# Kernel optimization log

Measured on AMD Instinct MI355X. Metric: run time of the kernel, lower is better.

The kernel has to match this reference:

```python
import jax, jax.numpy as jnp
import numpy as np

# ---- static hyperparameters (from init_kwargs) ----
N_ORDER = 3
P = N_ORDER + 1                      # nodes per element
N_ELEM = 64
N_NODES = N_ELEM * N_ORDER + 1       # 193
XMIN_IN, XMAX_IN = -1.0, 1.0         # inner layer domain
XMIN_OUT, XMAX_OUT = -3.0, 3.0       # outer layer domain (covers t_ik range)
N_SAMPLES, N_WIDTH, NDIM = 32768, 32, 4

_NODES = np.linspace(-1.0, 1.0, P)   # reference-element nodes


def lagr_bases(xt):
    """Lagrange basis values and 1st/2nd derivatives on the reference element.
    xt: (...,) -> phi, dphi, ddphi each (..., P)."""
    nd = _NODES
    d = xt[..., None] - jnp.asarray(nd, dtype=xt.dtype)  # (..., P), d[...,m] = x - nodes[m]
    phi_l, dphi_l, ddphi_l = [], [], []
    for j in range(P):
        # phi_j = prod_{m!=j} (x - n_m)/(n_j - n_m)
        p = jnp.ones_like(xt)
        for m in range(P):
            if m != j:
                p = p * d[..., m] / float(nd[j] - nd[m])
        phi_l.append(p)
        # dphi_j = sum_{i!=j} 1/(n_j-n_i) * prod_{m!=i,j} (x-n_m)/(n_j-n_m)
        y = jnp.zeros_like(xt)
        for i in range(P):
            if i == j:
                continue
            k = jnp.ones_like(xt) / float(nd[j] - nd[i])
            for m in range(P):
                if m != i and m != j:
                    k = k * d[..., m] / float(nd[j] - nd[m])
            y = y + k
        dphi_l.append(y)
        # ddphi_j = sum_{i!=j} 1/(n_j-n_i) * sum_{m!=i,j} 1/(n_j-n_m) * prod_{n!=i,j,m} (x-n_n)/(n_j-n_n)
        y2 = jnp.zeros_like(xt)
        for i in range(P):
            if i == j:
                continue
            ks = jnp.zeros_like(xt)
            for m in range(P):
                if m == i or m == j:
                    continue
                kp = jnp.ones_like(xt) / float(nd[j] - nd[m])
                for n in range(P):
                    if n != i and n != j and n != m:
                        kp = kp * d[..., n] / float(nd[j] - nd[n])
                ks = ks + kp
            y2 = y2 + ks / float(nd[j] - nd[i])
        ddphi_l.append(y2)
    return (jnp.stack(phi_l, -1), jnp.stack(dphi_l, -1), jnp.stack(ddphi_l, -1))


def layer_transform(x, x_min, x_max, n_nodes, n_elements):
    """Shift to natural coords, pick element by floor-division, map to reference coords."""
    x_shift = (n_nodes - 1) * (x - x_min) / (x_max - x_min)
    id_el = jnp.clip(jnp.floor(x_shift / N_ORDER), 0.0, n_elements - 1)
    nodes_l = (id_el * N_ORDER).astype(jnp.int32)
    x_ref = 2.0 * (x_shift - nodes_l) / N_ORDER - 1.0
    delta = 0.5 * N_ORDER * (x_max - x_min) / (n_nodes - 1)
    return x_ref, nodes_l, delta


def setup_inputs() -> dict:
    key = jax.random.key(0)
    k1, k2, k3 = jax.random.split(key, 3)
    x = jax.random.uniform(k1, (N_SAMPLES, NDIM), dtype=jnp.float32)       # in [x_min, x_max]
    W_in = 0.1 * jax.random.normal(k2, (N_WIDTH, N_NODES, NDIM), dtype=jnp.float32)
    W_out = 0.1 * jax.random.normal(k3, (N_WIDTH, N_NODES), dtype=jnp.float32)
    return {"x": x, "W_in": W_in, "W_out": W_out}


def reference(x, W_in, W_out):
    I, J = x.shape
    K = W_in.shape[0]
    # ---- inner layer: per-(sample,width,dim) local Lagrange basis ----
    xk = jnp.broadcast_to(x[:, None, :], (I, K, J))                        # (I,K,J)
    xt, nodes_l, delta = layer_transform(xk, XMIN_IN, XMAX_IN, N_NODES, N_ELEM)
    phi, dphi, ddphi = lagr_bases(xt)                                      # (I,K,J,P)
    # gather form of scatter + einsum('kpj,ikpj->ik'): sum_p,j W[k, nodes_l+p, j]*phi_local
    node_idx = nodes_l[..., None] + jnp.arange(P)                          # (I,K,J,P)
    kk = jnp.arange(K)[None, :, None, None]
    jj = jnp.arange(J)[None, None, :, None]
    Wg = W_in[kk, node_idx, jj]                                            # (I,K,J,P)
    t = jnp.einsum('ikjp,ikjp->ik', Wg, phi)
    dt = jnp.einsum('ikjp,ikjp->ik', Wg, dphi) / delta
    ddt = jnp.einsum('ikjp,ikjp->ik', Wg, ddphi) / (delta * delta)
    # ---- outer layer on t_ik (already 2D) ----
    xt2, nodes_l2, _ = layer_transform(t, XMIN_OUT, XMAX_OUT, N_NODES, N_ELEM)
    phi2, _, _ = lagr_bases(xt2)                                           # (I,K,P)
    node_idx2 = nodes_l2[..., None] + jnp.arange(P)                        # (I,K,P)
    kk2 = jnp.arange(K)[None, :, None]
    W2g = W_out[kk2, node_idx2]                                            # (I,K,P)
    y = jnp.einsum('ikp,ikp->ik', W2g, phi2)
    return jnp.stack([y, t, dt, ddt], axis=0)                              # (4,I,K)
```

## Files before the change

kernel.cpp:

```cpp
#include <hip/hip_runtime.h>

constexpr int I_SAMPLES = 32768;
constexpr int K_WIDTH   = 32;
constexpr int NNODES    = 193;
constexpr int N_ELEM    = 64;
constexpr int IK        = I_SAMPLES * K_WIDTH;

constexpr int W1_N = 4 * N_ELEM * K_WIDTH;
constexpr int W2_N = N_ELEM * K_WIDTH;

__global__ __launch_bounds__(256) void prep_kernel(
    const float* __restrict__ W_in,
    const float* __restrict__ W_out,
    float4* __restrict__ W1,
    float4* __restrict__ W2)
{
    const int t = blockIdx.x * blockDim.x + threadIdx.x;
    if (t < W1_N) {
        const int k = t & 31;
        const int e = (t >> 5) & 63;
        const int j = t >> 11;
        const int base = (k * NNODES + 3 * e) * 4 + j;
        float4 v;
        v.x = W_in[base + 0 * 4];
        v.y = W_in[base + 1 * 4];
        v.z = W_in[base + 2 * 4];
        v.w = W_in[base + 3 * 4];
        W1[t] = v;
    } else if (t < W1_N + W2_N) {
        const int u = t - W1_N;
        const int k = u & 31;
        const int e = u >> 5;
        const int base = k * NNODES + 3 * e;
        float4 v;
        v.x = W_out[base + 0];
        v.y = W_out[base + 1];
        v.z = W_out[base + 2];
        v.w = W_out[base + 3];
        W2[u] = v;
    }
}

__global__ __launch_bounds__(256) void kann_kernel(
    const float* __restrict__ x,
    const float4* __restrict__ W1,
    const float4* __restrict__ W2,
    float* __restrict__ out)
{
    const int tid = blockIdx.x * blockDim.x + threadIdx.x;
    const int c = tid & 7;
    const int i = tid >> 3;

    const float4 xv = reinterpret_cast<const float4*>(x)[i];
    const float xj[4] = {xv.x, xv.y, xv.z, xv.w};

    const float C3[4] = {-0.5625f,  1.6875f, -1.6875f,  0.5625f};
    const float C2[4] = { 0.5625f, -0.5625f, -0.5625f,  0.5625f};
    const float C1[4] = { 0.0625f, -1.6875f,  1.6875f, -0.0625f};
    const float C0[4] = {-0.0625f,  0.5625f,  0.5625f, -0.0625f};

    float tacc[4] = {0.f, 0.f, 0.f, 0.f};
    float dta[4]  = {0.f, 0.f, 0.f, 0.f};
    float dda[4]  = {0.f, 0.f, 0.f, 0.f};

    #pragma unroll
    for (int j = 0; j < 4; ++j) {
        const float xs = (192.0f * (xj[j] + 1.0f)) / 2.0f;
        float ide = floorf(xs / 3.0f);
        ide = fminf(fmaxf(ide, 0.0f), 63.0f);
        const int e  = (int)ide;
        const int nl = 3 * e;
        const float xr = (2.0f * (xs - (float)nl)) / 3.0f - 1.0f;

        float phi[4], dph[4], ddp[4];
        #pragma unroll
        for (int p = 0; p < 4; ++p) {
            phi[p] = ((C3[p] * xr + C2[p]) * xr + C1[p]) * xr + C0[p];
            dph[p] = (3.0f * C3[p] * xr + 2.0f * C2[p]) * xr + C1[p];
            ddp[p] = 6.0f * C3[p] * xr + 2.0f * C2[p];
        }

        const float4* row = W1 + (j * N_ELEM + e) * K_WIDTH + c;
        #pragma unroll
        for (int q = 0; q < 4; ++q) {
            const float4 w = row[8 * q];
            const float wv[4] = {w.x, w.y, w.z, w.w};
            #pragma unroll
            for (int p = 0; p < 4; ++p) {
                tacc[q] += wv[p] * phi[p];
                dta[q]  += wv[p] * dph[p];
                dda[q]  += wv[p] * ddp[p];
            }
        }
    }

    #pragma unroll
    for (int q = 0; q < 4; ++q) {
        const float t   = tacc[q];
        const float dt  = dta[q] * 64.0f;
        const float ddt = dda[q] * 4096.0f;

        const float xs2 = (192.0f * (t + 3.0f)) / 6.0f;
        float id2 = floorf(xs2 / 3.0f);
        id2 = fminf(fmaxf(id2, 0.0f), 63.0f);
        const int e2  = (int)id2;
        const int nl2 = 3 * e2;
        const float xr2 = (2.0f * (xs2 - (float)nl2)) / 3.0f - 1.0f;

        const int k = c + 8 * q;
        const float4 w2 = W2[e2 * K_WIDTH + k];
        const float w2v[4] = {w2.x, w2.y, w2.z, w2.w};
        float y = 0.f;
        #pragma unroll
        for (int p = 0; p < 4; ++p) {
            const float phi2 = ((C3[p] * xr2 + C2[p]) * xr2 + C1[p]) * xr2 + C0[p];
            y += w2v[p] * phi2;
        }

        const int o = i * K_WIDTH + k;
        out[o]          = y;
        out[IK + o]     = t;
        out[2 * IK + o] = dt;
        out[3 * IK + o] = ddt;
    }
}

extern "C" void kernel_launch(void* const* d_in, const int* in_sizes, int n_in,
                              void* d_out, int out_size, void* d_ws, size_t ws_size,
                              hipStream_t stream) {
    const float* x     = (const float*)d_in[0];
    const float* W_in  = (const float*)d_in[1];
    const float* W_out = (const float*)d_in[2];
    float* out = (float*)d_out;

    float4* W1 = (float4*)d_ws;
    float4* W2 = W1 + W1_N;

    prep_kernel<<<(W1_N + W2_N + 255) / 256, 256, 0, stream>>>(W_in, W_out, W1, W2);
    kann_kernel<<<(I_SAMPLES * 8) / 256, 256, 0, stream>>>(x, W1, W2, out);
}
```

Before: 70.34 us.

## Fuse weight prep into main kernel with swizzled LDS staging and float4 stores

After: 68.86 us. -2.1%, faster.

```diff
diff --git a/kernel.cpp b/kernel.cpp
--- a/kernel.cpp
+++ b/kernel.cpp
@@ -6,50 +6,48 @@
 constexpr int N_ELEM    = 64;
 constexpr int IK        = I_SAMPLES * K_WIDTH;
 
-constexpr int W1_N = 4 * N_ELEM * K_WIDTH;
-constexpr int W2_N = N_ELEM * K_WIDTH;
-
-__global__ __launch_bounds__(256) void prep_kernel(
+__global__ __launch_bounds__(512, 4) void kann_fused_kernel(
+    const float* __restrict__ x,
     const float* __restrict__ W_in,
     const float* __restrict__ W_out,
-    float4* __restrict__ W1,
-    float4* __restrict__ W2)
-{
-    const int t = blockIdx.x * blockDim.x + threadIdx.x;
-    if (t < W1_N) {
-        const int k = t & 31;
-        const int e = (t >> 5) & 63;
-        const int j = t >> 11;
-        const int base = (k * NNODES + 3 * e) * 4 + j;
-        float4 v;
-        v.x = W_in[base + 0 * 4];
-        v.y = W_in[base + 1 * 4];
-        v.z = W_in[base + 2 * 4];
-        v.w = W_in[base + 3 * 4];
-        W1[t] = v;
-    } else if (t < W1_N + W2_N) {
-        const int u = t - W1_N;
-        const int k = u & 31;
-        const int e = u >> 5;
-        const int base = k * NNODES + 3 * e;
-        float4 v;
-        v.x = W_out[base + 0];
-        v.y = W_out[base + 1];
-        v.z = W_out[base + 2];
-        v.w = W_out[base + 3];
-        W2[u] = v;
-    }
-}
-
-__global__ __launch_bounds__(256) void kann_kernel(
-    const float* __restrict__ x,
-    const float4* __restrict__ W1,
-    const float4* __restrict__ W2,
     float* __restrict__ out)
 {
-    const int tid = blockIdx.x * blockDim.x + threadIdx.x;
-    const int c = tid & 7;
-    const int i = tid >> 3;
+    __shared__ float lds_f[4 * 64 * 64];
+    float4* lds4 = reinterpret_cast<float4*>(lds_f);
+
+    const int khalf = blockIdx.x & 1;
+    const int sblk  = blockIdx.x >> 1;
+
+    {
+        const float4* Win4 = reinterpret_cast<const float4*>(W_in)
+                           + khalf * 16 * NNODES;
+        for (int s4 = threadIdx.x; s4 < 16 * NNODES; s4 += 512) {
+            const int kl = s4 / NNODES;
+            const int n  = s4 - kl * NNODES;
+            const float4 v = Win4[s4];
+            const float vj[4] = {v.x, v.y, v.z, v.w};
+            const int e  = n / 3;
+            const int t3 = n - 3 * e;
+            if (n < 192) {
+                const int w = (((kl ^ (e & 7)) << 2) + t3);
+                #pragma unroll
+                for (int j = 0; j < 4; ++j)
+                    lds_f[(j * 64 + e) * 64 + w] = vj[j];
+            }
+            if (t3 == 0 && n > 0) {
+                const int eb = e - 1;
+                const int w = (((kl ^ (eb & 7)) << 2) + 3);
+                #pragma unroll
+                for (int j = 0; j < 4; ++j)
+                    lds_f[(j * 64 + eb) * 64 + w] = vj[j];
+            }
+        }
+    }
+    __syncthreads();
+
+    const int c  = threadIdx.x & 3;
+    const int il = threadIdx.x >> 2;
+    const int i  = sblk * 128 + il;
 
     const float4 xv = reinterpret_cast<const float4*>(x)[i];
     const float xj[4] = {xv.x, xv.y, xv.z, xv.w};
@@ -80,25 +78,28 @@
             ddp[p] = 6.0f * C3[p] * xr + 2.0f * C2[p];
         }
 
-        const float4* row = W1 + (j * N_ELEM + e) * K_WIDTH + c;
+        const float4* row4 = lds4 + (j * 64 + e) * 16;
+        const int sw = e & 7;
         #pragma unroll
-        for (int q = 0; q < 4; ++q) {
-            const float4 w = row[8 * q];
+        for (int m = 0; m < 4; ++m) {
+            const int kl = 4 * c + m;
+            const float4 w = row4[kl ^ sw];
             const float wv[4] = {w.x, w.y, w.z, w.w};
             #pragma unroll
             for (int p = 0; p < 4; ++p) {
-                tacc[q] += wv[p] * phi[p];
-                dta[q]  += wv[p] * dph[p];
-                dda[q]  += wv[p] * ddp[p];
+                tacc[m] += wv[p] * phi[p];
+                dta[m]  += wv[p] * dph[p];
+                dda[m]  += wv[p] * ddp[p];
             }
         }
     }
 
+    float yo[4], to[4], dto[4], ddto[4];
     #pragma unroll
-    for (int q = 0; q < 4; ++q) {
-        const float t   = tacc[q];
-        const float dt  = dta[q] * 64.0f;
-        const float ddt = dda[q] * 4096.0f;
+    for (int m = 0; m < 4; ++m) {
+        const float t   = tacc[m];
+        const float dt  = dta[m] * 64.0f;
+        const float ddt = dda[m] * 4096.0f;
 
         const float xs2 = (192.0f * (t + 3.0f)) / 6.0f;
         float id2 = floorf(xs2 / 3.0f);
@@ -107,22 +108,23 @@
         const int nl2 = 3 * e2;
         const float xr2 = (2.0f * (xs2 - (float)nl2)) / 3.0f - 1.0f;
 
-        const int k = c + 8 * q;
-        const float4 w2 = W2[e2 * K_WIDTH + k];
-        const float w2v[4] = {w2.x, w2.y, w2.z, w2.w};
+        const int k = khalf * 16 + 4 * c + m;
+        const float* w2 = W_out + k * NNODES + nl2;
         float y = 0.f;
         #pragma unroll
         for (int p = 0; p < 4; ++p) {
             const float phi2 = ((C3[p] * xr2 + C2[p]) * xr2 + C1[p]) * xr2 + C0[p];
-            y += w2v[p] * phi2;
+            y += w2[p] * phi2;
         }
+        yo[m] = y; to[m] = t; dto[m] = dt; ddto[m] = ddt;
+    }
 
-        const int o = i * K_WIDTH + k;
-        out[o]          = y;
-        out[IK + o]     = t;
-        out[2 * IK + o] = dt;
-        out[3 * IK + o] = ddt;
-    }
+    float4* out4 = reinterpret_cast<float4*>(out);
+    const int ob = i * 8 + khalf * 4 + c;
+    out4[ob]              = make_float4(yo[0],   yo[1],   yo[2],   yo[3]);
+    out4[IK / 4 + ob]     = make_float4(to[0],   to[1],   to[2],   to[3]);
+    out4[2 * IK / 4 + ob] = make_float4(dto[0],  dto[1],  dto[2],  dto[3]);
+    out4[3 * IK / 4 + ob] = make_float4(ddto[0], ddto[1], ddto[2], ddto[3]);
 }
 
 extern "C" void kernel_launch(void* const* d_in, const int* in_sizes, int n_in,
@@ -133,9 +135,5 @@
     const float* W_out = (const float*)d_in[2];
     float* out = (float*)d_out;
 
-    float4* W1 = (float4*)d_ws;
-    float4* W2 = W1 + W1_N;
-
-    prep_kernel<<<(W1_N + W2_N + 255) / 256, 256, 0, stream>>>(W_in, W_out, W1, W2);
-    kann_kernel<<<(I_SAMPLES * 8) / 256, 256, 0, stream>>>(x, W1, W2, out);
+    kann_fused_kernel<<<512, 512, 0, stream>>>(x, W_in, W_out, out);
 }
```
